# Optimization experiments

Hardware: AMD Instinct MI355X
Metric: run time of the kernel (lower is better)

The kernel has to match this reference:

```python
import jax, jax.numpy as jnp
import numpy as np

D_MODEL = 1024
N_HEADS = 16
HEAD_DIM = D_MODEL // N_HEADS


def setup_inputs() -> dict:
    key = jax.random.key(0)
    k0, k1, k2, k3, k4, k5 = jax.random.split(key, 6)
    s = 1.0 / np.sqrt(D_MODEL)
    return {
        "q": jax.random.normal(k0, (2, 2048, D_MODEL), dtype=jnp.float32),
        "Wq": jax.random.normal(k1, (D_MODEL, D_MODEL), dtype=jnp.float32) * s,
        "Wk": jax.random.normal(k2, (D_MODEL, D_MODEL), dtype=jnp.float32) * s,
        "Wv": jax.random.normal(k3, (D_MODEL, D_MODEL), dtype=jnp.float32) * s,
        "Wo": jax.random.normal(k4, (D_MODEL, D_MODEL), dtype=jnp.float32) * s,
        "bo": jax.random.normal(k5, (D_MODEL,), dtype=jnp.float32) * 0.01,
    }


def _split_heads(x):
    b, s, _ = x.shape
    return x.reshape(b, s, N_HEADS, HEAD_DIM).transpose(0, 2, 1, 3)  # [b,h,s,d]


def reference(q, Wq, Wk, Wv, Wo, bo):
    # self-attention: k = v = q
    qh = _split_heads(q @ Wq)  # [b,h,s,d]
    kh = _split_heads(q @ Wk)
    vh = _split_heads(q @ Wv)
    scale = 1.0 / np.sqrt(HEAD_DIM).astype(np.float32)
    scores = jnp.einsum("bhqd,bhkd->bhqk", qh, kh) * scale
    attn = jax.nn.softmax(scores, axis=-1)
    ctx = jnp.einsum("bhqk,bhkd->bhqd", attn, vh)
    b, h, s, d = ctx.shape
    ctx = ctx.transpose(0, 2, 1, 3).reshape(b, s, h * d)
    return ctx @ Wo + bo
```

## Files before the change

### kernel.cpp

```cpp
#include <hip/hip_runtime.h>
#include <cstdint>

typedef unsigned short u16;
typedef __bf16 bf16x8 __attribute__((ext_vector_type(8)));
typedef __bf16 bf16x2 __attribute__((ext_vector_type(2)));
typedef float floatx4 __attribute__((ext_vector_type(4)));
typedef unsigned short u16x4 __attribute__((ext_vector_type(4)));
typedef unsigned short u16x8 __attribute__((ext_vector_type(8)));

#define MFMA16(a, b, c) __builtin_amdgcn_mfma_f32_16x16x32_bf16((a), (b), (c), 0, 0, 0)
#define QSCALE_LOG2E 0.18033688011112042f


typedef __attribute__((address_space(3))) void as3_void;
typedef __attribute__((address_space(1))) void as1_void;

static __device__ __forceinline__ void async_load16(const void* g, void* l) {
  __builtin_amdgcn_global_load_lds((as1_void*)(uintptr_t)g, (as3_void*)(uintptr_t)l,
                                   16, 0, 0);
}

static __device__ __forceinline__ u16 f2bf(float f) {
  union { float f; unsigned int u; } v; v.f = f;
  unsigned int u = v.u;
  u += 0x7fffu + ((u >> 16) & 1u);
  return (u16)(u >> 16);
}

static __device__ __forceinline__ u16x4 pack_bf4(float a, float b, float c, float d) {
#if __has_builtin(__builtin_amdgcn_cvt_pk_bf16_f32)
  union { u16x4 v4; bf16x2 v2[2]; } u;
  u.v2[0] = __builtin_amdgcn_cvt_pk_bf16_f32(a, b);
  u.v2[1] = __builtin_amdgcn_cvt_pk_bf16_f32(c, d);
  return u.v4;
#else
  u16x4 r; r[0] = f2bf(a); r[1] = f2bf(b); r[2] = f2bf(c); r[3] = f2bf(d);
  return r;
#endif
}

static __device__ __forceinline__ float fast_exp2(float x) {
#if __has_builtin(__builtin_amdgcn_exp2f)
  return __builtin_amdgcn_exp2f(x);
#else
  return exp2f(x);
#endif
}


__global__ __launch_bounds__(256) void prep_kernel(
    const float* __restrict__ w0, const float* __restrict__ w1,
    const float* __restrict__ w2, const float* __restrict__ w3,
    u16* __restrict__ wout,
    const float* __restrict__ xin, u16* __restrict__ xout) {
  if (blockIdx.z == 4) {
    int blk = blockIdx.y * 16 + blockIdx.x;
    size_t base = (size_t)blk * 16384 + (size_t)threadIdx.x * 8;
#pragma unroll
    for (int r = 0; r < 8; r++) {
      size_t i = base + (size_t)r * 2048;
      float4 a = *(const float4*)(xin + i);
      float4 b = *(const float4*)(xin + i + 4);
      u16x8 o;
      o[0] = f2bf(a.x); o[1] = f2bf(a.y); o[2] = f2bf(a.z); o[3] = f2bf(a.w);
      o[4] = f2bf(b.x); o[5] = f2bf(b.y); o[6] = f2bf(b.z); o[7] = f2bf(b.w);
      *(u16x8*)(xout + i) = o;
    }
    return;
  }
  __shared__ u16 t[64][65];
  const float* in = (blockIdx.z == 0) ? w0 : (blockIdx.z == 1) ? w1
                    : (blockIdx.z == 2) ? w2 : w3;
  u16* oz = wout + (size_t)blockIdx.z * (1024 * 1024);
  const int tid = threadIdx.x;
  const int x = tid & 63, y0 = tid >> 6;
  const int bx = blockIdx.x * 64, by = blockIdx.y * 64;
#pragma unroll
  for (int p = 0; p < 16; p++) {
    int y = y0 + p * 4;
    t[y][x] = f2bf(in[(size_t)(by + y) * 1024 + bx + x]);
  }
  __syncthreads();
#pragma unroll
  for (int p = 0; p < 16; p++) {
    int r = y0 + p * 4;
    oz[(size_t)(bx + r) * 1024 + by + x] = t[x][r];
  }
}


__global__ __launch_bounds__(256, 3) void gemm_qkv_kernel(
    const u16* __restrict__ A, const u16* __restrict__ BT,
    u16* __restrict__ out, u16* __restrict__ outVT) {
  __shared__ u16 As[128 * 32];
  __shared__ u16 Bs[128 * 32];
  __shared__ u16 tb[64 * 136];
  const int tid = threadIdx.x;
  const int w = tid >> 6, lane = tid & 63;
  const int bm = blockIdx.y * 128, bn = blockIdx.x * 128;
  const int z = blockIdx.z;
  const int K = 1024, N = 1024;
  const u16* Bz = BT + (size_t)z * N * K;

  const int c0 = w * 2, c1 = c0 + 1;
  const int mA0 = c0 * 16 + (lane >> 2), mA1 = c1 * 16 + (lane >> 2);
  const int kg0 = (lane & 3) ^ ((mA0 >> 1) & 3);
  const int kg1 = (lane & 3) ^ ((mA1 >> 1) & 3);
  const u16* agp0 = A + (size_t)(bm + mA0) * K + kg0 * 8;
  const u16* agp1 = A + (size_t)(bm + mA1) * K + kg1 * 8;
  const u16* bgp0 = Bz + (size_t)(bn + mA0) * K + kg0 * 8;
  const u16* bgp1 = Bz + (size_t)(bn + mA1) * K + kg1 * 8;
  u16* ald0 = As + c0 * 512; u16* ald1 = As + c1 * 512;
  u16* bld0 = Bs + c0 * 512; u16* bld1 = Bs + c1 * 512;

  const int wm = (w >> 1) * 64, wn = (w & 1) * 64;
  floatx4 acc[4][4] = {};

  int a_off[4], b_off[4];
#pragma unroll
  for (int i = 0; i < 4; i++) {
    int m = wm + i * 16 + (lane & 15);
    a_off[i] = m * 32 + (((lane >> 4) ^ ((m >> 1) & 3)) * 8);
    int n = wn + i * 16 + (lane & 15);
    b_off[i] = n * 32 + (((lane >> 4) ^ ((n >> 1) & 3)) * 8);
  }

  for (int k0 = 0; k0 < K; k0 += 32) {
    __syncthreads();
    async_load16(agp0 + k0, ald0);
    async_load16(agp1 + k0, ald1);
    async_load16(bgp0 + k0, bld0);
    async_load16(bgp1 + k0, bld1);
    __syncthreads();
    bf16x8 af[4], bf[4];
#pragma unroll
    for (int i = 0; i < 4; i++) af[i] = *(const bf16x8*)(As + a_off[i]);
#pragma unroll
    for (int j = 0; j < 4; j++) bf[j] = *(const bf16x8*)(Bs + b_off[j]);
#pragma unroll
    for (int i = 0; i < 4; i++)
#pragma unroll
      for (int j = 0; j < 4; j++)
        acc[i][j] = MFMA16(af[i], bf[j], acc[i][j]);
  }

  const int roff = (lane >> 4) * 4;
  const int coff = lane & 15;
  if (z == 2) {
    const int b = bm >> 11, s0 = bm & 2047;
#pragma unroll
    for (int half = 0; half < 2; half++) {
      __syncthreads();
      if ((w & 1) == half) {
#pragma unroll
        for (int i = 0; i < 4; i++) {
          int s_local = wm + i * 16 + roff;
#pragma unroll
          for (int j = 0; j < 4; j++) {
            int c_local = j * 16 + coff;
            u16x4 pk = pack_bf4(acc[i][j][0], acc[i][j][1],
                                acc[i][j][2], acc[i][j][3]);
            *(u16x4*)(tb + c_local * 136 + s_local) = pk;
          }
        }
      }
      __syncthreads();
#pragma unroll
      for (int p = 0; p < 4; p++) {
        int c_local = (tid >> 4) & 15;
        int row = p * 16 + c_local;
        int so = tid & 15;
        int cg = bn + half * 64 + row;
        int h = cg >> 6, d = cg & 63;
        u16x8 vv = *(const u16x8*)(tb + row * 136 + so * 8);
        *(u16x8*)(outVT + ((size_t)(b * 16 + h) * 64 + d) * 2048 + s0 + so * 8) = vv;
      }
    }
  } else {
    const float sc = (z == 0) ? QSCALE_LOG2E : 1.0f;
    u16* outz = out + (size_t)z * 4096 * 1024;
#pragma unroll
    for (int i = 0; i < 4; i++) {
      int r0 = bm + wm + i * 16 + roff;
#pragma unroll
      for (int j = 0; j < 4; j++) {
        int c = bn + wn + j * 16 + coff;
#pragma unroll
        for (int r = 0; r < 4; r++)
          outz[(size_t)(r0 + r) * N + c] = f2bf(acc[i][j][r] * sc);
      }
    }
  }
}


__global__ __launch_bounds__(256, 2) void gemm_o_kernel(
    const u16* __restrict__ A, const u16* __restrict__ BT,
    const float* __restrict__ bias, float* __restrict__ out) {
  __shared__ u16 As[128 * 32];
  __shared__ u16 Bs[64 * 32];
  const int tid = threadIdx.x;
  const int w = tid >> 6, lane = tid & 63;
  const int bm = blockIdx.y * 128, bn = blockIdx.x * 64;
  const int K = 1024, N = 1024;

  const u16* gp[3]; u16* ld[3];
#pragma unroll
  for (int i = 0; i < 3; i++) {
    int c = w * 3 + i;
    if (c < 8) {
      int m = c * 16 + (lane >> 2);
      int kg = (lane & 3) ^ ((m >> 1) & 3);
      gp[i] = A + (size_t)(bm + m) * K + kg * 8;
      ld[i] = As + c * 512;
    } else {
      int cb = c - 8;
      int n = cb * 16 + (lane >> 2);
      int kg = (lane & 3) ^ ((n >> 1) & 3);
      gp[i] = BT + (size_t)(bn + n) * K + kg * 8;
      ld[i] = Bs + cb * 512;
    }
  }

  const int wm = (w >> 1) * 64, wn = (w & 1) * 32;
  floatx4 acc[4][2] = {};

  int a_off[4], b_off[2];
#pragma unroll
  for (int i = 0; i < 4; i++) {
    int m = wm + i * 16 + (lane & 15);
    a_off[i] = m * 32 + (((lane >> 4) ^ ((m >> 1) & 3)) * 8);
  }
#pragma unroll
  for (int j = 0; j < 2; j++) {
    int n = wn + j * 16 + (lane & 15);
    b_off[j] = n * 32 + (((lane >> 4) ^ ((n >> 1) & 3)) * 8);
  }

  for (int k0 = 0; k0 < K; k0 += 32) {
    __syncthreads();
    async_load16(gp[0] + k0, ld[0]);
    async_load16(gp[1] + k0, ld[1]);
    async_load16(gp[2] + k0, ld[2]);
    __syncthreads();
    bf16x8 af[4], bf[2];
#pragma unroll
    for (int i = 0; i < 4; i++) af[i] = *(const bf16x8*)(As + a_off[i]);
#pragma unroll
    for (int j = 0; j < 2; j++) bf[j] = *(const bf16x8*)(Bs + b_off[j]);
#pragma unroll
    for (int i = 0; i < 4; i++)
#pragma unroll
      for (int j = 0; j < 2; j++)
        acc[i][j] = MFMA16(af[i], bf[j], acc[i][j]);
  }

  const int roff = (lane >> 4) * 4;
  const int coff = lane & 15;
#pragma unroll
  for (int i = 0; i < 4; i++) {
    int r0 = bm + wm + i * 16 + roff;
#pragma unroll
    for (int j = 0; j < 2; j++) {
      int c = bn + wn + j * 16 + coff;
      float bv = bias[c];
#pragma unroll
      for (int r = 0; r < 4; r++)
        out[(size_t)(r0 + r) * N + c] = acc[i][j][r] + bv;
    }
  }
}


__global__ __launch_bounds__(256, 2) void attn_kernel(
    const u16* __restrict__ Q, const u16* __restrict__ Kx,
    const u16* __restrict__ VT, u16* __restrict__ ctx) {
  __shared__ __align__(16) u16 lds[8192 + 8192 + 4 * 64 * 68];
  u16* Ks = lds;
  u16* Vs = lds + 8192;
  u16* Ps = lds + 16384;
  const int tid = threadIdx.x;
  const int w = tid >> 6, lane = tid & 63;
  const int qh = w >> 1, sh = w & 1;
  const int bid = blockIdx.x;
  const int bh = (bid >> 7) * 8 + (bid & 7);
  const int q0 = ((bid >> 3) & 15) * 128;
  const int b = bh >> 4, h = bh & 15;
  const u16* Qh = Q + (size_t)b * 2048 * 1024 + h * 64;
  const u16* Kh = Kx + (size_t)b * 2048 * 1024 + h * 64;
  const u16* Vh = VT + (size_t)bh * 64 * 2048;
  const int quad = lane >> 4;

  const int qbase = q0 + qh * 64;
  bf16x8 qf[4][2];
#pragma unroll
  for (int qt = 0; qt < 4; qt++)
#pragma unroll
    for (int ks = 0; ks < 2; ks++)
      qf[qt][ks] = *(const bf16x8*)(Qh + (size_t)(qbase + qt * 16 + (lane & 15)) * 1024 +
                                    ks * 32 + quad * 8);

  bf16x8 onesf;
#pragma unroll
  for (int i = 0; i < 8; i++) onesf[i] = (__bf16)1.0f;
  const floatx4 zero4 = {};

  const u16* kgp[4]; const u16* vgp[4];
  u16* kld[4]; u16* vld[4];
#pragma unroll
  for (int i = 0; i < 4; i++) {
    int c = w * 4 + i;
    int sl = c * 8 + (lane >> 3);
    int dg = (lane & 7) ^ (lane >> 3);
    kgp[i] = Kh + (size_t)sl * 1024 + dg * 8;
    kld[i] = Ks + c * 512;
    int dl = c * 4 + quad;
    int sg = (lane & 15) ^ (dl & 15);
    vgp[i] = Vh + (size_t)dl * 2048 + sg * 8;
    vld[i] = Vs + c * 512;
  }

  const int slot_k0 = quad ^ (lane & 7);
  const int slot_k1 = (4 + quad) ^ (lane & 7);
  const u16* kf0_base = Ks + sh * 4096 + (lane & 15) * 64 + slot_k0 * 8;
  const u16* kf1_base = Ks + sh * 4096 + (lane & 15) * 64 + slot_k1 * 8;

  floatx4 o[4][4] = {};
  floatx4 lacc[4] = {};
  u16* Pw = Ps + w * (64 * 68);
  int qrow[4];
#pragma unroll
  for (int qt = 0; qt < 4; qt++) qrow[qt] = (qt * 16 + (lane & 15)) * 68;

  for (int t = 0; t < 16; t++) {
    const size_t k0 = (size_t)t * 128;
    __syncthreads();
#pragma unroll
    for (int i = 0; i < 4; i++) {
      async_load16(kgp[i] + k0 * 1024, kld[i]);
      async_load16(vgp[i] + k0, vld[i]);
    }
    __syncthreads();

    floatx4 st[4][4];
#pragma unroll
    for (int si = 0; si < 4; si++) {
      bf16x8 kf0 = *(const bf16x8*)(kf0_base + si * 1024);
      bf16x8 kf1 = *(const bf16x8*)(kf1_base + si * 1024);
#pragma unroll
      for (int qt = 0; qt < 4; qt++)
        st[si][qt] = MFMA16(kf1, qf[qt][1], MFMA16(kf0, qf[qt][0], zero4));
    }
#pragma unroll
    for (int si = 0; si < 4; si++)
#pragma unroll
      for (int qt = 0; qt < 4; qt++) {
        u16x4 pk = pack_bf4(fast_exp2(st[si][qt][0]), fast_exp2(st[si][qt][1]),
                            fast_exp2(st[si][qt][2]), fast_exp2(st[si][qt][3]));
        *(u16x4*)(Pw + qrow[qt] + si * 16 + quad * 4) = pk;
      }

#pragma unroll
    for (int ksl = 0; ksl < 2; ksl++) {
      int kb = sh * 2 + ksl;
      bf16x8 vf[4];
#pragma unroll
      for (int jt = 0; jt < 4; jt++) {
        int d = jt * 16 + (lane & 15);
        int slot = (kb * 4 + quad) ^ (d & 15);
        vf[jt] = *(const bf16x8*)(Vs + d * 128 + slot * 8);
      }
#pragma unroll
      for (int qt = 0; qt < 4; qt++) {
        bf16x8 pf = *(const bf16x8*)(Pw + qrow[qt] + ksl * 32 + quad * 8);
#pragma unroll
        for (int jt = 0; jt < 4; jt++)
          o[qt][jt] = MFMA16(pf, vf[jt], o[qt][jt]);
        lacc[qt] = MFMA16(pf, onesf, lacc[qt]);
      }
    }
  }

  __syncthreads();
  floatx4* dump  = (floatx4*)lds;
  floatx4* ldump = (floatx4*)(lds + 16384);
  if (sh == 1) {
    int base = qh * 1024;
#pragma unroll
    for (int qt = 0; qt < 4; qt++)
#pragma unroll
      for (int jt = 0; jt < 4; jt++)
        dump[base + (qt * 4 + jt) * 64 + lane] = o[qt][jt];
#pragma unroll
    for (int i = 0; i < 4; i++)
      ldump[qh * 256 + i * 64 + lane] = lacc[i];
  }
  __syncthreads();
  if (sh == 0) {
    int base = qh * 1024;
#pragma unroll
    for (int qt = 0; qt < 4; qt++)
#pragma unroll
      for (int jt = 0; jt < 4; jt++)
        o[qt][jt] += dump[base + (qt * 4 + jt) * 64 + lane];
#pragma unroll
    for (int i = 0; i < 4; i++)
      lacc[i] += ldump[qh * 256 + i * 64 + lane];
#pragma unroll
    for (int qt = 0; qt < 4; qt++)
#pragma unroll
      for (int r = 0; r < 4; r++) {
        float inv = 1.0f / lacc[qt][r];
        int s = qbase + qt * 16 + quad * 4 + r;
#pragma unroll
        for (int j = 0; j < 4; j++) {
          int c = h * 64 + j * 16 + (lane & 15);
          ctx[(size_t)(b * 2048 + s) * 1024 + c] = f2bf(o[qt][j][r] * inv);
        }
      }
  }
}


extern "C" void kernel_launch(void* const* d_in, const int* in_sizes, int n_in,
                              void* d_out, int out_size, void* d_ws, size_t ws_size,
                              hipStream_t stream) {
  (void)in_sizes; (void)n_in; (void)out_size; (void)ws_size;
  const float* x  = (const float*)d_in[0];
  const float* Wq = (const float*)d_in[1];
  const float* Wk = (const float*)d_in[2];
  const float* Wv = (const float*)d_in[3];
  const float* Wo = (const float*)d_in[4];
  const float* bo = (const float*)d_in[5];
  u16* ws = (u16*)d_ws;
  const size_t MM = 1024 * 1024;
  u16* WT  = ws;
  u16* WoT = ws + 3 * MM;
  u16* Xb  = ws + 4 * MM;
  u16* QKV = ws + 8 * MM;
  u16* VTp = ws + 20 * MM;
  u16* CTX = ws + 24 * MM;

  dim3 blk(256);
  prep_kernel<<<dim3(16, 16, 5), blk, 0, stream>>>(Wq, Wk, Wv, Wo, WT, x, Xb);
  gemm_qkv_kernel<<<dim3(8, 32, 3), blk, 0, stream>>>(Xb, WT, QKV, VTp);
  attn_kernel<<<dim3(512, 1, 1), blk, 0, stream>>>(QKV, QKV + 4 * MM, VTp, CTX);
  gemm_o_kernel<<<dim3(16, 32, 1), blk, 0, stream>>>(CTX, WoT, bo, (float*)d_out);
}
```

Measured before the change: 196.2 us.

## Split attention block into 8 waves with 32 query rows each

The attention kernel now runs 512 threads (8 waves) per block instead of 256. Each wave pair handles 32 query rows rather than 64, and each wave loads only half as many K/V chunks per tile. The P scratch buffer is restructured to 32x72 per wave. The aim is to cut registers per wave (fewer accumulators) and raise the number of resident waves, improving latency hiding. The cost is more waves contending on the same barriers and each K fragment being reused across fewer query tiles.

```diff
diff --git a/kernel.cpp b/kernel.cpp
--- a/kernel.cpp
+++ b/kernel.cpp
@@ -272,16 +272,17 @@
 }
 
 
-__global__ __launch_bounds__(256, 2) void attn_kernel(
+__global__ __launch_bounds__(512, 4) void attn_kernel(
     const u16* __restrict__ Q, const u16* __restrict__ Kx,
     const u16* __restrict__ VT, u16* __restrict__ ctx) {
-  __shared__ __align__(16) u16 lds[8192 + 8192 + 4 * 64 * 68];
+  __shared__ __align__(16) u16 lds[8192 + 8192 + 8 * 32 * 72];
   u16* Ks = lds;
   u16* Vs = lds + 8192;
   u16* Ps = lds + 16384;
   const int tid = threadIdx.x;
   const int w = tid >> 6, lane = tid & 63;
-  const int qh = w >> 1, sh = w & 1;
+  const int qq = w >> 1, sh = w & 1;
+  const int quad = lane >> 4;
   const int bid = blockIdx.x;
   const int bh = (bid >> 7) * 8 + (bid & 7);
   const int q0 = ((bid >> 3) & 15) * 128;
@@ -289,12 +290,11 @@
   const u16* Qh = Q + (size_t)b * 2048 * 1024 + h * 64;
   const u16* Kh = Kx + (size_t)b * 2048 * 1024 + h * 64;
   const u16* Vh = VT + (size_t)bh * 64 * 2048;
-  const int quad = lane >> 4;
-
-  const int qbase = q0 + qh * 64;
-  bf16x8 qf[4][2];
-#pragma unroll
-  for (int qt = 0; qt < 4; qt++)
+
+  const int qbase = q0 + qq * 32;
+  bf16x8 qf[2][2];
+#pragma unroll
+  for (int qt = 0; qt < 2; qt++)
 #pragma unroll
     for (int ks = 0; ks < 2; ks++)
       qf[qt][ks] = *(const bf16x8*)(Qh + (size_t)(qbase + qt * 16 + (lane & 15)) * 1024 +
@@ -305,11 +305,11 @@
   for (int i = 0; i < 8; i++) onesf[i] = (__bf16)1.0f;
   const floatx4 zero4 = {};
 
-  const u16* kgp[4]; const u16* vgp[4];
-  u16* kld[4]; u16* vld[4];
-#pragma unroll
-  for (int i = 0; i < 4; i++) {
-    int c = w * 4 + i;
+  const u16* kgp[2]; const u16* vgp[2];
+  u16* kld[2]; u16* vld[2];
+#pragma unroll
+  for (int i = 0; i < 2; i++) {
+    int c = w * 2 + i;
     int sl = c * 8 + (lane >> 3);
     int dg = (lane & 7) ^ (lane >> 3);
     kgp[i] = Kh + (size_t)sl * 1024 + dg * 8;
@@ -325,40 +325,40 @@
   const u16* kf0_base = Ks + sh * 4096 + (lane & 15) * 64 + slot_k0 * 8;
   const u16* kf1_base = Ks + sh * 4096 + (lane & 15) * 64 + slot_k1 * 8;
 
-  floatx4 o[4][4] = {};
-  floatx4 lacc[4] = {};
-  u16* Pw = Ps + w * (64 * 68);
-  int qrow[4];
-#pragma unroll
-  for (int qt = 0; qt < 4; qt++) qrow[qt] = (qt * 16 + (lane & 15)) * 68;
+  floatx4 o[2][4] = {};
+  floatx4 lacc[2] = {};
+  u16* Pw = Ps + w * (32 * 72);
+  const int qrow0 = (lane & 15) * 72;
+  const int qrow1 = (16 + (lane & 15)) * 72;
 
   for (int t = 0; t < 16; t++) {
     const size_t k0 = (size_t)t * 128;
     __syncthreads();
 #pragma unroll
-    for (int i = 0; i < 4; i++) {
+    for (int i = 0; i < 2; i++) {
       async_load16(kgp[i] + k0 * 1024, kld[i]);
       async_load16(vgp[i] + k0, vld[i]);
     }
     __syncthreads();
 
-    floatx4 st[4][4];
+    floatx4 st[4][2];
 #pragma unroll
     for (int si = 0; si < 4; si++) {
       bf16x8 kf0 = *(const bf16x8*)(kf0_base + si * 1024);
       bf16x8 kf1 = *(const bf16x8*)(kf1_base + si * 1024);
 #pragma unroll
-      for (int qt = 0; qt < 4; qt++)
+      for (int qt = 0; qt < 2; qt++)
         st[si][qt] = MFMA16(kf1, qf[qt][1], MFMA16(kf0, qf[qt][0], zero4));
     }
 #pragma unroll
-    for (int si = 0; si < 4; si++)
-#pragma unroll
-      for (int qt = 0; qt < 4; qt++) {
-        u16x4 pk = pack_bf4(fast_exp2(st[si][qt][0]), fast_exp2(st[si][qt][1]),
-                            fast_exp2(st[si][qt][2]), fast_exp2(st[si][qt][3]));
-        *(u16x4*)(Pw + qrow[qt] + si * 16 + quad * 4) = pk;
-      }
+    for (int si = 0; si < 4; si++) {
+      u16x4 pk0 = pack_bf4(fast_exp2(st[si][0][0]), fast_exp2(st[si][0][1]),
+                           fast_exp2(st[si][0][2]), fast_exp2(st[si][0][3]));
+      u16x4 pk1 = pack_bf4(fast_exp2(st[si][1][0]), fast_exp2(st[si][1][1]),
+                           fast_exp2(st[si][1][2]), fast_exp2(st[si][1][3]));
+      *(u16x4*)(Pw + qrow0 + si * 16 + quad * 4) = pk0;
+      *(u16x4*)(Pw + qrow1 + si * 16 + quad * 4) = pk1;
+    }
 
 #pragma unroll
     for (int ksl = 0; ksl < 2; ksl++) {
@@ -371,8 +371,9 @@
         vf[jt] = *(const bf16x8*)(Vs + d * 128 + slot * 8);
       }
 #pragma unroll
-      for (int qt = 0; qt < 4; qt++) {
-        bf16x8 pf = *(const bf16x8*)(Pw + qrow[qt] + ksl * 32 + quad * 8);
+      for (int qt = 0; qt < 2; qt++) {
+        bf16x8 pf = *(const bf16x8*)(Pw + (qt * 16 + (lane & 15)) * 72 +
+                                     ksl * 32 + quad * 8);
 #pragma unroll
         for (int jt = 0; jt < 4; jt++)
           o[qt][jt] = MFMA16(pf, vf[jt], o[qt][jt]);
@@ -385,29 +386,29 @@
   floatx4* dump  = (floatx4*)lds;
   floatx4* ldump = (floatx4*)(lds + 16384);
   if (sh == 1) {
-    int base = qh * 1024;
-#pragma unroll
-    for (int qt = 0; qt < 4; qt++)
+    int base = qq * 512;
+#pragma unroll
+    for (int qt = 0; qt < 2; qt++)
 #pragma unroll
       for (int jt = 0; jt < 4; jt++)
         dump[base + (qt * 4 + jt) * 64 + lane] = o[qt][jt];
 #pragma unroll
-    for (int i = 0; i < 4; i++)
-      ldump[qh * 256 + i * 64 + lane] = lacc[i];
+    for (int qt = 0; qt < 2; qt++)
+      ldump[qq * 128 + qt * 64 + lane] = lacc[qt];
   }
   __syncthreads();
   if (sh == 0) {
-    int base = qh * 1024;
-#pragma unroll
-    for (int qt = 0; qt < 4; qt++)
+    int base = qq * 512;
+#pragma unroll
+    for (int qt = 0; qt < 2; qt++)
 #pragma unroll
       for (int jt = 0; jt < 4; jt++)
         o[qt][jt] += dump[base + (qt * 4 + jt) * 64 + lane];
 #pragma unroll
-    for (int i = 0; i < 4; i++)
-      lacc[i] += ldump[qh * 256 + i * 64 + lane];
-#pragma unroll
-    for (int qt = 0; qt < 4; qt++)
+    for (int qt = 0; qt < 2; qt++)
+      lacc[qt] += ldump[qq * 128 + qt * 64 + lane];
+#pragma unroll
+    for (int qt = 0; qt < 2; qt++)
 #pragma unroll
       for (int r = 0; r < 4; r++) {
         float inv = 1.0f / lacc[qt][r];
@@ -444,6 +445,6 @@
   dim3 blk(256);
   prep_kernel<<<dim3(16, 16, 5), blk, 0, stream>>>(Wq, Wk, Wv, Wo, WT, x, Xb);
   gemm_qkv_kernel<<<dim3(8, 32, 3), blk, 0, stream>>>(Xb, WT, QKV, VTp);
-  attn_kernel<<<dim3(512, 1, 1), blk, 0, stream>>>(QKV, QKV + 4 * MM, VTp, CTX);
+  attn_kernel<<<dim3(512, 1, 1), dim3(512), 0, stream>>>(QKV, QKV + 4 * MM, VTp, CTX);
   gemm_o_kernel<<<dim3(16, 32, 1), blk, 0, stream>>>(CTX, WoT, bo, (float*)d_out);
 }
```

Result: faster. 184.5 us (-6.0%).
